# Optimization experiments

Measured on AMD Instinct MI355X. Metric: run time of the kernel, lower is better.

Reference implementation:

```python
import jax, jax.numpy as jnp
import numpy as np

D = 512
H = 8
DH = D // H


def setup_inputs() -> dict:
    key = jax.random.key(0)
    ks = jax.random.split(key, 6)
    B, S = 2, 4096
    scale = 1.0 / np.sqrt(D)
    x = jax.random.normal(ks[0], (B, S, D), dtype=jnp.float32)
    W_q = jax.random.normal(ks[1], (D, D), dtype=jnp.float32) * scale
    W_k = jax.random.normal(ks[2], (D, D), dtype=jnp.float32) * scale
    W_v = jax.random.normal(ks[3], (D, D), dtype=jnp.float32) * scale
    W_proj = jax.random.normal(ks[4], (D, D), dtype=jnp.float32) * scale
    b_proj = jax.random.normal(ks[5], (D,), dtype=jnp.float32) * 0.01
    return {"x": x, "W_q": W_q, "W_k": W_k, "W_v": W_v,
            "W_proj": W_proj, "b_proj": b_proj}


def reference(x, W_q, W_k, W_v, W_proj, b_proj):
    B, S, _ = x.shape
    # torch Linear: y = x @ W.T
    def proj(W):
        y = jnp.einsum('bsd,ed->bse', x, W)
        return y.reshape(B, S, H, DH).transpose(0, 2, 1, 3)  # [B,H,S,DH]
    q, k, v = proj(W_q), proj(W_k), proj(W_v)
    scores = jnp.einsum('bhqd,bhkd->bhqk', q, k) / np.sqrt(DH)  # [B,H,S,S]
    causal = jnp.tril(jnp.ones((S, S), dtype=bool))
    neg = jnp.finfo(scores.dtype).min
    scores = jnp.where(causal[None, None, :, :], scores, neg)
    w = jax.nn.softmax(scores, axis=-1)
    attn = jnp.einsum('bhqk,bhkd->bhqd', w, v)  # [B,H,S,DH]
    attn = attn.transpose(0, 2, 1, 3).reshape(B, S, D)
    return jnp.einsum('bsd,ed->bse', attn, W_proj) + b_proj
```

## Files before the change

kernel.cpp:

```cpp
#include <hip/hip_runtime.h>
#include <hip/hip_bf16.h>
#include <stdint.h>

#define D_MODEL 512
#define NH 8
#define DH 64
#define SEQ 4096
#define NBH 16
#define NX  (2 * SEQ * D_MODEL)
#define NW  (D_MODEL * D_MODEL)

typedef __attribute__((ext_vector_type(8))) short bf16x8;
typedef __attribute__((ext_vector_type(4))) float f32x4;
typedef __attribute__((ext_vector_type(16))) float f32x16;

#define CSCALE 0.18033688011112042f

__device__ __forceinline__ uint32_t pkbf(float a, float b) {
    uint32_t r;
    asm("v_cvt_pk_bf16_f32 %0, %1, %2" : "=v"(r) : "v"(a), "v"(b));
    return r;
}

#define SWZ(R) (((R) + ((R) >> 2)) & 3)

#define BAR() do {                                          \
    asm volatile("s_waitcnt lgkmcnt(0)" ::: "memory");      \
    __builtin_amdgcn_s_barrier();                           \
} while (0)

#define BARC(N) do {                                                     \
    asm volatile("s_waitcnt vmcnt(" #N ") lgkmcnt(0)" ::: "memory");     \
    __builtin_amdgcn_s_barrier();                                        \
} while (0)

typedef const __attribute__((address_space(1))) void* gvp;
typedef __attribute__((address_space(3))) void* lvp;
__device__ __forceinline__ void gload16(const short* g, short* l) {
    __builtin_amdgcn_global_load_lds((gvp)g, (lvp)l, 16, 0, 0);
}

__device__ __forceinline__ bf16x8 cvt8(float4 u, float4 v, float s) {
    union { uint32_t w[4]; bf16x8 h; } r;
    r.w[0] = pkbf(u.x * s, u.y * s); r.w[1] = pkbf(u.z * s, u.w * s);
    r.w[2] = pkbf(v.x * s, v.y * s); r.w[3] = pkbf(v.z * s, v.w * s);
    return r.h;
}

__global__ __launch_bounds__(256) void cvt_pre(
    const float* __restrict__ x,
    const float* __restrict__ Wq, const float* __restrict__ Wk,
    const float* __restrict__ Wv, const float* __restrict__ Wp,
    short* __restrict__ xb, short* __restrict__ Wb)
{
    const size_t t = ((size_t)blockIdx.x * 256 + threadIdx.x) * 8;
    const float* src; short* dst; float s = 1.0f; size_t off;
    if (t < NX) {
        src = x; dst = xb; off = t;
    } else {
        const size_t u = t - NX;
        const int w = (int)(u >> 18);
        off = u & (NW - 1);
        src = (w == 0) ? Wq : (w == 1) ? Wk : (w == 2) ? Wv : Wp;
        dst = Wb + ((size_t)w << 18);
        s = (w == 0) ? CSCALE : 1.0f;
    }
    float4 a = *(const float4*)(src + off);
    float4 b = *(const float4*)(src + off + 4);
    *(bf16x8*)(dst + off) = cvt8(a, b, s);
}

__global__ __launch_bounds__(256) void qkv_kernel(
    const short* __restrict__ xb, const short* __restrict__ Wb,
    short* __restrict__ Qb, short* __restrict__ Kb, short* __restrict__ Vt)
{
    __shared__ __align__(16) short at[3][4096];
    __shared__ __align__(16) short bt[3][4096];

    const int tid  = threadIdx.x;
    const int wave = tid >> 6;
    const int lane = tid & 63;
    const int ln = lane & 15, quad = lane >> 4;
    const int z = blockIdx.z;
    const short* W = Wb + ((size_t)z << 18);
    const int m0 = blockIdx.x * 128;
    const int n0 = blockIdx.y * 128;
    const int mh = (wave & 1) * 64, nh = (wave >> 1) * 64;

    const int ck0 = tid, ck1 = tid + 256;
    const int R0 = ck0 >> 2, R1 = ck1 >> 2;
    const int c0 = (ck0 & 3) ^ SWZ(R0), c1 = (ck1 & 3) ^ SWZ(R1);
    const int lbase = (tid & 192) * 8;

    auto stage = [&](int buf, int kc) {
        const short* gA0 = xb + (size_t)(m0 + R0) * D_MODEL + kc + c0 * 8;
        const short* gA1 = xb + (size_t)(m0 + R1) * D_MODEL + kc + c1 * 8;
        const short* gB0 = W + (size_t)(n0 + R0) * D_MODEL + kc + c0 * 8;
        const short* gB1 = W + (size_t)(n0 + R1) * D_MODEL + kc + c1 * 8;
        gload16(gA0, &at[buf][lbase]);
        gload16(gA1, &at[buf][lbase] + 2048);
        gload16(gB0, &bt[buf][lbase]);
        gload16(gB1, &bt[buf][lbase] + 2048);
    };

    f32x4 acc[4][4] = {};

    stage(0, 0);
    stage(1, 32);

    for (int s = 0; s < 16; ++s) {
        const int cur = s % 3;
        if (s == 15) BARC(0); else BARC(4);
        if (s < 14) stage((s + 2) % 3, (s + 2) * 32);

        bf16x8 a[4], b[4];
#pragma unroll
        for (int i = 0; i < 4; ++i) {
            const int R = mh + i * 16 + ln;
            a[i] = *(const bf16x8*)(&at[cur][R * 32 + ((quad ^ SWZ(R)) * 8)]);
        }
#pragma unroll
        for (int j = 0; j < 4; ++j) {
            const int R = nh + j * 16 + ln;
            b[j] = *(const bf16x8*)(&bt[cur][R * 32 + ((quad ^ SWZ(R)) * 8)]);
        }
        __builtin_amdgcn_s_setprio(1);
#pragma unroll
        for (int i = 0; i < 4; ++i)
#pragma unroll
            for (int j = 0; j < 4; ++j)
                acc[i][j] = __builtin_amdgcn_mfma_f32_16x16x32_bf16(
                    a[i], b[j], acc[i][j], 0, 0, 0);
        __builtin_amdgcn_s_setprio(0);
    }

    if (z == 2) {
#pragma unroll
        for (int i = 0; i < 4; ++i) {
            const int row0 = m0 + mh + i * 16 + quad * 4;
            const int bb = row0 >> 12, sq = row0 & (SEQ - 1);
#pragma unroll
            for (int j = 0; j < 4; ++j) {
                const int n = n0 + nh + j * 16 + ln;
                const int h = n >> 6, dh = n & 63;
                uint2 st;
                st.x = pkbf(acc[i][j][0], acc[i][j][1]);
                st.y = pkbf(acc[i][j][2], acc[i][j][3]);
                *(uint2*)(Vt + (size_t)((bb * NH + h) * DH + dh) * SEQ + sq) = st;
            }
        }
    } else {
        short* P = (z == 0) ? Qb : Kb;
#pragma unroll
        for (int i = 0; i < 4; ++i)
#pragma unroll
            for (int j = 0; j < 4; ++j) {
                const int n = n0 + nh + j * 16 + ln;
                const int h = n >> 6, dh = n & 63;
                const uint32_t lo = pkbf(acc[i][j][0], acc[i][j][1]);
                const uint32_t hi2 = pkbf(acc[i][j][2], acc[i][j][3]);
#pragma unroll
                for (int r = 0; r < 4; ++r) {
                    const int row = m0 + mh + i * 16 + quad * 4 + r;
                    const int bb = row >> 12, sq = row & (SEQ - 1);
                    const uint32_t w = (r < 2) ? lo : hi2;
                    P[((size_t)((bb * NH + h) * SEQ + sq) << 6) + dh] =
                        (short)((r & 1) ? (w >> 16) : (w & 0xffff));
                }
            }
    }
}

__global__ __launch_bounds__(256) void attn_kernel(
    const short* __restrict__ Qb, const short* __restrict__ Kb,
    const short* __restrict__ Vt, short* __restrict__ ao)
{
    __shared__ __align__(16) short kt[2][4096];
    __shared__ __align__(16) short vt[2][4096];

    const int tid  = threadIdx.x;
    const int wave = tid >> 6;
    const int lane = tid & 63;
    const int l31 = lane & 31, hi = lane >> 5;
    const int bh = blockIdx.y;
    const int w_ = (blockIdx.x + 4 * bh) & 31;
    const int g2 = ((bh >> 3) & 1) ? (31 - w_) : w_;
    const short* Qp = Qb + (size_t)bh * SEQ * DH;
    const short* Kp = Kb + (size_t)bh * SEQ * DH;
    const short* Vp = Vt + (size_t)bh * DH * SEQ;
    const int bb = bh >> 3, h = bh & 7;
    const int q0 = g2 * 128 + wave * 32;
    const int myq = q0 + l31;
    const int jdiag = q0 >> 6;
    const int jmax = 2 * g2 + 1;

    const int ckA = tid, ckB = tid + 256;
    const int RA = ckA >> 3, RB = ckB >> 3;
    const int cA = (ckA & 7) ^ (RA & 7), cB = (ckB & 7) ^ (RB & 7);
    const int RA31 = RA & 31, RB31 = RB & 31;
    const int kkA = (RA & 32) + ((RA31 & 8) << 1) + ((RA31 & 4) << 1)
                  + ((RA31 & 16) >> 2) + (RA31 & 3);
    const int kkB = (RB & 32) + ((RB31 & 8) << 1) + ((RB31 & 4) << 1)
                  + ((RB31 & 16) >> 2) + (RB31 & 3);
    const size_t kOffA = ((size_t)kkA << 6) + cA * 8;
    const size_t kOffB = ((size_t)kkB << 6) + cB * 8;
    const size_t vOffA = (size_t)RA * SEQ + cA * 8;
    const size_t vOffB = (size_t)RB * SEQ + cB * 8;

    bf16x8 sk0, sk1, sv0, sv1;
    auto load_tile = [&](int j) {
        const size_t k0 = (size_t)j * 64;
        sk0 = *(const bf16x8*)(Kp + (k0 << 6) + kOffA);
        sk1 = *(const bf16x8*)(Kp + (k0 << 6) + kOffB);
        sv0 = *(const bf16x8*)(Vp + vOffA + k0);
        sv1 = *(const bf16x8*)(Vp + vOffB + k0);
    };
    auto write_tile = [&](int buf) {
        *(bf16x8*)&kt[buf][ckA * 8] = sk0;
        *(bf16x8*)&kt[buf][ckB * 8] = sk1;
        *(bf16x8*)&vt[buf][ckA * 8] = sv0;
        *(bf16x8*)&vt[buf][ckB * 8] = sv1;
    };

    bf16x8 qf[4];
#pragma unroll
    for (int c = 0; c < 4; ++c)
        qf[c] = *(const bf16x8*)(Qp + (size_t)myq * DH + c * 16 + hi * 8);

    const bf16x8 ones = { (short)0x3F80, (short)0x3F80, (short)0x3F80,
                          (short)0x3F80, (short)0x3F80, (short)0x3F80,
                          (short)0x3F80, (short)0x3F80 };

    f32x16 o0 = {}, o1 = {};
    f32x16 lacc = {};

    load_tile(0);
    write_tile(0);
    load_tile(1);
    BAR();

    for (int j = 0; j <= jmax; ++j) {
        const int cur = j & 1;
        if (j < jmax) {
            write_tile(cur ^ 1);
            if (j + 1 < jmax) load_tile(j + 2);
        }

        if ((j << 6) <= q0 + 31) {
            f32x16 s0 = {}, s1 = {};
            const int sw = l31 & 7;
            __builtin_amdgcn_s_setprio(1);
#pragma unroll
            for (int c = 0; c < 4; ++c) {
                const int pc = ((2 * c + hi) ^ sw) * 8;
                bf16x8 a0 = *(const bf16x8*)(&kt[cur][l31 * 64 + pc]);
                bf16x8 a1 = *(const bf16x8*)(&kt[cur][(32 + l31) * 64 + pc]);
                s0 = __builtin_amdgcn_mfma_f32_32x32x16_bf16(a0, qf[c], s0, 0, 0, 0);
                s1 = __builtin_amdgcn_mfma_f32_32x32x16_bf16(a1, qf[c], s1, 0, 0, 0);
            }
            __builtin_amdgcn_s_setprio(0);
            if (j >= jdiag) {
                const int k0 = j * 64;
#pragma unroll
                for (int reg = 0; reg < 16; ++reg) {
                    const int kl = ((reg >> 2) & 1) * 16 + hi * 8
                                 + ((reg >> 3) & 1) * 4 + (reg & 3);
                    if (k0 + kl > myq)      s0[reg] = -3e38f;
                    if (k0 + 32 + kl > myq) s1[reg] = -3e38f;
                }
            }
#pragma unroll
            for (int i = 0; i < 16; ++i) {
                s0[i] = __builtin_amdgcn_exp2f(s0[i]);
                s1[i] = __builtin_amdgcn_exp2f(s1[i]);
            }

            union { uint32_t u[4]; bf16x8 v; } p00, p01, p10, p11;
            p00.u[0] = pkbf(s0[0], s0[1]);   p00.u[1] = pkbf(s0[2], s0[3]);
            p00.u[2] = pkbf(s0[8], s0[9]);   p00.u[3] = pkbf(s0[10], s0[11]);
            p01.u[0] = pkbf(s0[4], s0[5]);   p01.u[1] = pkbf(s0[6], s0[7]);
            p01.u[2] = pkbf(s0[12], s0[13]); p01.u[3] = pkbf(s0[14], s0[15]);
            p10.u[0] = pkbf(s1[0], s1[1]);   p10.u[1] = pkbf(s1[2], s1[3]);
            p10.u[2] = pkbf(s1[8], s1[9]);   p10.u[3] = pkbf(s1[10], s1[11]);
            p11.u[0] = pkbf(s1[4], s1[5]);   p11.u[1] = pkbf(s1[6], s1[7]);
            p11.u[2] = pkbf(s1[12], s1[13]); p11.u[3] = pkbf(s1[14], s1[15]);

            __builtin_amdgcn_s_setprio(1);
            lacc = __builtin_amdgcn_mfma_f32_32x32x16_bf16(ones, p00.v, lacc, 0, 0, 0);
            lacc = __builtin_amdgcn_mfma_f32_32x32x16_bf16(ones, p01.v, lacc, 0, 0, 0);
            lacc = __builtin_amdgcn_mfma_f32_32x32x16_bf16(ones, p10.v, lacc, 0, 0, 0);
            lacc = __builtin_amdgcn_mfma_f32_32x32x16_bf16(ones, p11.v, lacc, 0, 0, 0);

            {
                const short* vrow = &vt[cur][l31 * 64];
                bf16x8 v00 = *(const bf16x8*)(vrow + (((0 + hi) ^ sw) * 8));
                bf16x8 v01 = *(const bf16x8*)(vrow + (((2 + hi) ^ sw) * 8));
                bf16x8 v10 = *(const bf16x8*)(vrow + (((4 + hi) ^ sw) * 8));
                bf16x8 v11 = *(const bf16x8*)(vrow + (((6 + hi) ^ sw) * 8));
                o0 = __builtin_amdgcn_mfma_f32_32x32x16_bf16(v00, p00.v, o0, 0, 0, 0);
                o0 = __builtin_amdgcn_mfma_f32_32x32x16_bf16(v01, p01.v, o0, 0, 0, 0);
                o0 = __builtin_amdgcn_mfma_f32_32x32x16_bf16(v10, p10.v, o0, 0, 0, 0);
                o0 = __builtin_amdgcn_mfma_f32_32x32x16_bf16(v11, p11.v, o0, 0, 0, 0);
            }
            {
                const short* vrow = &vt[cur][(32 + l31) * 64];
                bf16x8 v00 = *(const bf16x8*)(vrow + (((0 + hi) ^ sw) * 8));
                bf16x8 v01 = *(const bf16x8*)(vrow + (((2 + hi) ^ sw) * 8));
                bf16x8 v10 = *(const bf16x8*)(vrow + (((4 + hi) ^ sw) * 8));
                bf16x8 v11 = *(const bf16x8*)(vrow + (((6 + hi) ^ sw) * 8));
                o1 = __builtin_amdgcn_mfma_f32_32x32x16_bf16(v00, p00.v, o1, 0, 0, 0);
                o1 = __builtin_amdgcn_mfma_f32_32x32x16_bf16(v01, p01.v, o1, 0, 0, 0);
                o1 = __builtin_amdgcn_mfma_f32_32x32x16_bf16(v10, p10.v, o1, 0, 0, 0);
                o1 = __builtin_amdgcn_mfma_f32_32x32x16_bf16(v11, p11.v, o1, 0, 0, 0);
            }
            __builtin_amdgcn_s_setprio(0);
        }
        BAR();
    }
    const float inv = 1.0f / lacc[0];
    short* orow = ao + (size_t)(bb * SEQ + myq) * D_MODEL + h * DH;
#pragma unroll
    for (int c = 0; c < 4; ++c) {
        uint2 st;
        st.x = pkbf(o0[4 * c] * inv,     o0[4 * c + 1] * inv);
        st.y = pkbf(o0[4 * c + 2] * inv, o0[4 * c + 3] * inv);
        *(uint2*)(orow + 8 * c + 4 * hi) = st;
    }
#pragma unroll
    for (int c = 0; c < 4; ++c) {
        uint2 st;
        st.x = pkbf(o1[4 * c] * inv,     o1[4 * c + 1] * inv);
        st.y = pkbf(o1[4 * c + 2] * inv, o1[4 * c + 3] * inv);
        *(uint2*)(orow + 32 + 8 * c + 4 * hi) = st;
    }
}

__global__ __launch_bounds__(256) void proj_kernel(
    const short* __restrict__ attn, const short* __restrict__ Wpb,
    const float* __restrict__ bias, float* __restrict__ out)
{
    __shared__ __align__(16) short at[3][2048];
    __shared__ __align__(16) short bt[3][4096];

    const int tid  = threadIdx.x;
    const int wave = tid >> 6;
    const int lane = tid & 63;
    const int ln = lane & 15, quad = lane >> 4;
    const int m0 = blockIdx.x * 64;
    const int n0 = blockIdx.y * 128;
    const int mh = (wave & 1) * 32, nh = (wave >> 1) * 64;

    const int RA = tid >> 2, cAc = (tid & 3) ^ SWZ(RA);
    const int ck0 = tid, ck1 = tid + 256;
    const int R0 = ck0 >> 2, R1 = ck1 >> 2;
    const int c0 = (ck0 & 3) ^ SWZ(R0), c1 = (ck1 & 3) ^ SWZ(R1);
    const int lbase = (tid & 192) * 8;

    auto stage = [&](int buf, int kc) {
        const short* gA = attn + (size_t)(m0 + RA) * D_MODEL + kc + cAc * 8;
        const short* gB0 = Wpb + (size_t)(n0 + R0) * D_MODEL + kc + c0 * 8;
        const short* gB1 = Wpb + (size_t)(n0 + R1) * D_MODEL + kc + c1 * 8;
        gload16(gA, &at[buf][lbase]);
        gload16(gB0, &bt[buf][lbase]);
        gload16(gB1, &bt[buf][lbase] + 2048);
    };

    f32x4 acc[2][4] = {};

    stage(0, 0);
    stage(1, 32);

    for (int s = 0; s < 16; ++s) {
        const int cur = s % 3;
        if (s == 15) BARC(0); else BARC(3);
        if (s < 14) stage((s + 2) % 3, (s + 2) * 32);

        bf16x8 a[2], b[4];
#pragma unroll
        for (int i = 0; i < 2; ++i) {
            const int R = mh + i * 16 + ln;
            a[i] = *(const bf16x8*)(&at[cur][R * 32 + ((quad ^ SWZ(R)) * 8)]);
        }
#pragma unroll
        for (int j = 0; j < 4; ++j) {
            const int R = nh + j * 16 + ln;
            b[j] = *(const bf16x8*)(&bt[cur][R * 32 + ((quad ^ SWZ(R)) * 8)]);
        }
        __builtin_amdgcn_s_setprio(1);
#pragma unroll
        for (int i = 0; i < 2; ++i)
#pragma unroll
            for (int j = 0; j < 4; ++j)
                acc[i][j] = __builtin_amdgcn_mfma_f32_16x16x32_bf16(
                    a[i], b[j], acc[i][j], 0, 0, 0);
        __builtin_amdgcn_s_setprio(0);
    }
#pragma unroll
    for (int j = 0; j < 4; ++j) {
        const int n = n0 + nh + j * 16 + ln;
        const float bv = bias[n];
#pragma unroll
        for (int i = 0; i < 2; ++i)
#pragma unroll
            for (int r = 0; r < 4; ++r) {
                const int row = m0 + mh + i * 16 + quad * 4 + r;
                out[(size_t)row * D_MODEL + n] = acc[i][j][r] + bv;
            }
    }
}

extern "C" void kernel_launch(void* const* d_in, const int* in_sizes, int n_in,
                              void* d_out, int out_size, void* d_ws, size_t ws_size,
                              hipStream_t stream) {
    const float* x  = (const float*)d_in[0];
    const float* Wq = (const float*)d_in[1];
    const float* Wk = (const float*)d_in[2];
    const float* Wv = (const float*)d_in[3];
    const float* Wp = (const float*)d_in[4];
    const float* bp = (const float*)d_in[5];
    float* out = (float*)d_out;

    short* Qb = (short*)d_ws;
    short* Kb = Qb + (size_t)NBH * SEQ * DH;
    short* Vt = Kb + (size_t)NBH * SEQ * DH;
    short* ab = Vt + (size_t)NBH * SEQ * DH;
    short* Wb = ab + (size_t)NBH * SEQ * DH;

    short* xb = (short*)d_out;

    cvt_pre<<<dim3((NX + 4 * NW) / (8 * 256)), 256, 0, stream>>>(
        x, Wq, Wk, Wv, Wp, xb, Wb);
    qkv_kernel<<<dim3(64, 4, 3), 256, 0, stream>>>(xb, Wb, Qb, Kb, Vt);
    attn_kernel<<<dim3(32, NBH), 256, 0, stream>>>(Qb, Kb, Vt, ab);
    proj_kernel<<<dim3(128, 4), 256, 0, stream>>>(ab, Wb + 3 * (size_t)NW, bp, out);
}
```

Baseline: 168.2 us.

## Merge paired query blocks into 512-thread attention blocks sharing K/V tiles

Attention blocks grow from 4 to 8 waves, each block covering two consecutive 128-query groups of one head. The K/V tiles staged in shared memory are reused by both groups, and each thread now loads one chunk instead of two. The intent is to halve global K/V traffic and load instructions per query. In exchange, the lower query group keeps iterating up to the upper group's causal limit, so its waves may stall at barriers or do masked work. The old reversed-ordering scheme used to balance causal work across blocks is dropped.

Measured after the change: 170.3 us. About the same (+1.3%).

```diff
diff --git a/kernel.cpp b/kernel.cpp
--- a/kernel.cpp
+++ b/kernel.cpp
@@ -171,7 +171,7 @@
     }
 }
 
-__global__ __launch_bounds__(256) void attn_kernel(
+__global__ __launch_bounds__(512) void attn_kernel(
     const short* __restrict__ Qb, const short* __restrict__ Kb,
     const short* __restrict__ Vt, short* __restrict__ ao)
 {
@@ -182,44 +182,39 @@
     const int wave = tid >> 6;
     const int lane = tid & 63;
     const int l31 = lane & 31, hi = lane >> 5;
-    const int bh = blockIdx.y;
-    const int w_ = (blockIdx.x + 4 * bh) & 31;
-    const int g2 = ((bh >> 3) & 1) ? (31 - w_) : w_;
+
+    const int bid = blockIdx.x + (blockIdx.y << 4);
+    const int bh  = bid & 15;
+    const int cp  = bid >> 4;
     const short* Qp = Qb + (size_t)bh * SEQ * DH;
     const short* Kp = Kb + (size_t)bh * SEQ * DH;
     const short* Vp = Vt + (size_t)bh * DH * SEQ;
     const int bb = bh >> 3, h = bh & 7;
-    const int q0 = g2 * 128 + wave * 32;
+
+    const int g2 = 2 * cp + (wave >> 2);
+    const int cw = wave & 3;
+    const int q0 = g2 * 128 + cw * 32;
     const int myq = q0 + l31;
     const int jdiag = q0 >> 6;
-    const int jmax = 2 * g2 + 1;
-
-    const int ckA = tid, ckB = tid + 256;
-    const int RA = ckA >> 3, RB = ckB >> 3;
-    const int cA = (ckA & 7) ^ (RA & 7), cB = (ckB & 7) ^ (RB & 7);
-    const int RA31 = RA & 31, RB31 = RB & 31;
+    const int jmax = 4 * cp + 3;
+
+    const int RA = tid >> 3;
+    const int cA = (tid & 7) ^ (RA & 7);
+    const int RA31 = RA & 31;
     const int kkA = (RA & 32) + ((RA31 & 8) << 1) + ((RA31 & 4) << 1)
                   + ((RA31 & 16) >> 2) + (RA31 & 3);
-    const int kkB = (RB & 32) + ((RB31 & 8) << 1) + ((RB31 & 4) << 1)
-                  + ((RB31 & 16) >> 2) + (RB31 & 3);
     const size_t kOffA = ((size_t)kkA << 6) + cA * 8;
-    const size_t kOffB = ((size_t)kkB << 6) + cB * 8;
     const size_t vOffA = (size_t)RA * SEQ + cA * 8;
-    const size_t vOffB = (size_t)RB * SEQ + cB * 8;
-
-    bf16x8 sk0, sk1, sv0, sv1;
+
+    bf16x8 sk0, sv0;
     auto load_tile = [&](int j) {
         const size_t k0 = (size_t)j * 64;
         sk0 = *(const bf16x8*)(Kp + (k0 << 6) + kOffA);
-        sk1 = *(const bf16x8*)(Kp + (k0 << 6) + kOffB);
         sv0 = *(const bf16x8*)(Vp + vOffA + k0);
-        sv1 = *(const bf16x8*)(Vp + vOffB + k0);
     };
     auto write_tile = [&](int buf) {
-        *(bf16x8*)&kt[buf][ckA * 8] = sk0;
-        *(bf16x8*)&kt[buf][ckB * 8] = sk1;
-        *(bf16x8*)&vt[buf][ckA * 8] = sv0;
-        *(bf16x8*)&vt[buf][ckB * 8] = sv1;
+        *(bf16x8*)&kt[buf][tid * 8] = sk0;
+        *(bf16x8*)&vt[buf][tid * 8] = sv0;
     };
 
     bf16x8 qf[4];
@@ -431,6 +426,6 @@
     cvt_pre<<<dim3((NX + 4 * NW) / (8 * 256)), 256, 0, stream>>>(
         x, Wq, Wk, Wv, Wp, xb, Wb);
     qkv_kernel<<<dim3(64, 4, 3), 256, 0, stream>>>(xb, Wb, Qb, Kb, Vt);
-    attn_kernel<<<dim3(32, NBH), 256, 0, stream>>>(Qb, Kb, Vt, ab);
+    attn_kernel<<<dim3(16, NBH), 512, 0, stream>>>(Qb, Kb, Vt, ab);
     proj_kernel<<<dim3(128, 4), 256, 0, stream>>>(ab, Wb + 3 * (size_t)NW, bp, out);
 }
```

## Fuse four pipeline stages into one persistent cooperative kernel with grid syncs

Applied to the files above, without the earlier changes.

Replaces four separate kernel launches (convert, QKV GEMM, attention, projection) with a single cooperative persistent kernel of 512 blocks that runs each stage in turn, separated by grid-wide syncs and sharing one LDS buffer. The goal is to remove launch overhead and inter-kernel gaps. In exchange, the grid size is fixed at 512 blocks, so the QKV stage needs two passes over its 768 tiles and the load is uneven, and grid.sync adds its own cost. If the cooperative launch fails, the code falls back to the original four launches.

Result: slower. 361.0 us (+114.6%).

```diff
diff --git a/kernel.cpp b/kernel.cpp
--- a/kernel.cpp
+++ b/kernel.cpp
@@ -1,6 +1,9 @@
 #include <hip/hip_runtime.h>
 #include <hip/hip_bf16.h>
+#include <hip/hip_cooperative_groups.h>
 #include <stdint.h>
+
+namespace cg = cooperative_groups;
 
 #define D_MODEL 512
 #define NH 8
@@ -47,13 +50,11 @@
     return r.h;
 }
 
-__global__ __launch_bounds__(256) void cvt_pre(
-    const float* __restrict__ x,
-    const float* __restrict__ Wq, const float* __restrict__ Wk,
-    const float* __restrict__ Wv, const float* __restrict__ Wp,
-    short* __restrict__ xb, short* __restrict__ Wb)
-{
-    const size_t t = ((size_t)blockIdx.x * 256 + threadIdx.x) * 8;
+
+__device__ __forceinline__ void cvt_body(
+    size_t t, const float* x, const float* Wq, const float* Wk,
+    const float* Wv, const float* Wp, short* xb, short* Wb)
+{
     const float* src; short* dst; float s = 1.0f; size_t off;
     if (t < NX) {
         src = x; dst = xb; off = t;
@@ -70,21 +71,16 @@
     *(bf16x8*)(dst + off) = cvt8(a, b, s);
 }
 
-__global__ __launch_bounds__(256) void qkv_kernel(
-    const short* __restrict__ xb, const short* __restrict__ Wb,
-    short* __restrict__ Qb, short* __restrict__ Kb, short* __restrict__ Vt)
-{
-    __shared__ __align__(16) short at[3][4096];
-    __shared__ __align__(16) short bt[3][4096];
-
-    const int tid  = threadIdx.x;
+__device__ __forceinline__ void qkv_body(
+    int m0, int n0, int z, int tid,
+    const short* xb, const short* Wb,
+    short* Qb, short* Kb, short* Vt,
+    short (*at)[4096], short (*bt)[4096])
+{
     const int wave = tid >> 6;
     const int lane = tid & 63;
     const int ln = lane & 15, quad = lane >> 4;
-    const int z = blockIdx.z;
     const short* W = Wb + ((size_t)z << 18);
-    const int m0 = blockIdx.x * 128;
-    const int n0 = blockIdx.y * 128;
     const int mh = (wave & 1) * 64, nh = (wave >> 1) * 64;
 
     const int ck0 = tid, ck1 = tid + 256;
@@ -171,20 +167,14 @@
     }
 }
 
-__global__ __launch_bounds__(256) void attn_kernel(
-    const short* __restrict__ Qb, const short* __restrict__ Kb,
-    const short* __restrict__ Vt, short* __restrict__ ao)
-{
-    __shared__ __align__(16) short kt[2][4096];
-    __shared__ __align__(16) short vt[2][4096];
-
-    const int tid  = threadIdx.x;
+__device__ __forceinline__ void attn_body(
+    int bh, int g2, int tid,
+    const short* Qb, const short* Kb, const short* Vt, short* ao,
+    short* kt0, short* vt0)
+{
     const int wave = tid >> 6;
     const int lane = tid & 63;
     const int l31 = lane & 31, hi = lane >> 5;
-    const int bh = blockIdx.y;
-    const int w_ = (blockIdx.x + 4 * bh) & 31;
-    const int g2 = ((bh >> 3) & 1) ? (31 - w_) : w_;
     const short* Qp = Qb + (size_t)bh * SEQ * DH;
     const short* Kp = Kb + (size_t)bh * SEQ * DH;
     const short* Vp = Vt + (size_t)bh * DH * SEQ;
@@ -216,10 +206,10 @@
         sv1 = *(const bf16x8*)(Vp + vOffB + k0);
     };
     auto write_tile = [&](int buf) {
-        *(bf16x8*)&kt[buf][ckA * 8] = sk0;
-        *(bf16x8*)&kt[buf][ckB * 8] = sk1;
-        *(bf16x8*)&vt[buf][ckA * 8] = sv0;
-        *(bf16x8*)&vt[buf][ckB * 8] = sv1;
+        *(bf16x8*)&kt0[buf * 4096 + ckA * 8] = sk0;
+        *(bf16x8*)&kt0[buf * 4096 + ckB * 8] = sk1;
+        *(bf16x8*)&vt0[buf * 4096 + ckA * 8] = sv0;
+        *(bf16x8*)&vt0[buf * 4096 + ckB * 8] = sv1;
     };
 
     bf16x8 qf[4];
@@ -253,8 +243,8 @@
 #pragma unroll
             for (int c = 0; c < 4; ++c) {
                 const int pc = ((2 * c + hi) ^ sw) * 8;
-                bf16x8 a0 = *(const bf16x8*)(&kt[cur][l31 * 64 + pc]);
-                bf16x8 a1 = *(const bf16x8*)(&kt[cur][(32 + l31) * 64 + pc]);
+                bf16x8 a0 = *(const bf16x8*)(&kt0[cur * 4096 + l31 * 64 + pc]);
+                bf16x8 a1 = *(const bf16x8*)(&kt0[cur * 4096 + (32 + l31) * 64 + pc]);
                 s0 = __builtin_amdgcn_mfma_f32_32x32x16_bf16(a0, qf[c], s0, 0, 0, 0);
                 s1 = __builtin_amdgcn_mfma_f32_32x32x16_bf16(a1, qf[c], s1, 0, 0, 0);
             }
@@ -292,7 +282,7 @@
             lacc = __builtin_amdgcn_mfma_f32_32x32x16_bf16(ones, p11.v, lacc, 0, 0, 0);
 
             {
-                const short* vrow = &vt[cur][l31 * 64];
+                const short* vrow = &vt0[cur * 4096 + l31 * 64];
                 bf16x8 v00 = *(const bf16x8*)(vrow + (((0 + hi) ^ sw) * 8));
                 bf16x8 v01 = *(const bf16x8*)(vrow + (((2 + hi) ^ sw) * 8));
                 bf16x8 v10 = *(const bf16x8*)(vrow + (((4 + hi) ^ sw) * 8));
@@ -303,7 +293,7 @@
                 o0 = __builtin_amdgcn_mfma_f32_32x32x16_bf16(v11, p11.v, o0, 0, 0, 0);
             }
             {
-                const short* vrow = &vt[cur][(32 + l31) * 64];
+                const short* vrow = &vt0[cur * 4096 + (32 + l31) * 64];
                 bf16x8 v00 = *(const bf16x8*)(vrow + (((0 + hi) ^ sw) * 8));
                 bf16x8 v01 = *(const bf16x8*)(vrow + (((2 + hi) ^ sw) * 8));
                 bf16x8 v10 = *(const bf16x8*)(vrow + (((4 + hi) ^ sw) * 8));
@@ -335,19 +325,14 @@
     }
 }
 
-__global__ __launch_bounds__(256) void proj_kernel(
-    const short* __restrict__ attn, const short* __restrict__ Wpb,
-    const float* __restrict__ bias, float* __restrict__ out)
-{
-    __shared__ __align__(16) short at[3][2048];
-    __shared__ __align__(16) short bt[3][4096];
-
-    const int tid  = threadIdx.x;
+__device__ __forceinline__ void proj_body(
+    int m0, int n0, int tid,
+    const short* ab, const short* Wpb, const float* bias, float* out,
+    short (*at)[2048], short (*bt)[4096])
+{
     const int wave = tid >> 6;
     const int lane = tid & 63;
     const int ln = lane & 15, quad = lane >> 4;
-    const int m0 = blockIdx.x * 64;
-    const int n0 = blockIdx.y * 128;
     const int mh = (wave & 1) * 32, nh = (wave >> 1) * 64;
 
     const int RA = tid >> 2, cAc = (tid & 3) ^ SWZ(RA);
@@ -357,7 +342,7 @@
     const int lbase = (tid & 192) * 8;
 
     auto stage = [&](int buf, int kc) {
-        const short* gA = attn + (size_t)(m0 + RA) * D_MODEL + kc + cAc * 8;
+        const short* gA = ab + (size_t)(m0 + RA) * D_MODEL + kc + cAc * 8;
         const short* gB0 = Wpb + (size_t)(n0 + R0) * D_MODEL + kc + c0 * 8;
         const short* gB1 = Wpb + (size_t)(n0 + R1) * D_MODEL + kc + c1 * 8;
         gload16(gA, &at[buf][lbase]);
@@ -407,6 +392,88 @@
                 out[(size_t)row * D_MODEL + n] = acc[i][j][r] + bv;
             }
     }
+}
+
+__global__ __launch_bounds__(256) void fused_kernel(
+    const float* x, const float* Wq, const float* Wk,
+    const float* Wv, const float* Wp, const float* bias,
+    short* xb, short* Wb, short* Qb, short* Kb, short* Vt,
+    short* ab, float* out)
+{
+    __shared__ __align__(16) short lds[24576];
+
+    cg::grid_group grid = cg::this_grid();
+    const int b   = blockIdx.x;
+    const int tid = threadIdx.x;
+
+    for (int i = 0; i < 5; ++i)
+        cvt_body(((size_t)(i * 512 + b) * 256 + tid) * 8,
+                 x, Wq, Wk, Wv, Wp, xb, Wb);
+    grid.sync();
+
+    for (int item = b; item < 768; item += 512) {
+        BAR();
+        qkv_body((item & 63) * 128, ((item >> 6) & 3) * 128, item >> 8,
+                 tid, xb, Wb, Qb, Kb, Vt,
+                 (short(*)[4096])lds, (short(*)[4096])(lds + 12288));
+    }
+    grid.sync();
+
+    {
+        const int bh = b >> 5;
+        const int w_ = ((b & 31) + 4 * bh) & 31;
+        const int g2 = ((bh >> 3) & 1) ? (31 - w_) : w_;
+        BAR();
+        attn_body(bh, g2, tid, Qb, Kb, Vt, ab, lds, lds + 8192);
+    }
+    grid.sync();
+
+    BAR();
+    proj_body((b >> 2) * 64, (b & 3) * 128, tid, ab, Wb + 3 * (size_t)NW,
+              bias, out,
+              (short(*)[2048])lds, (short(*)[4096])(lds + 6144));
+}
+
+__global__ __launch_bounds__(256) void cvt_pre(
+    const float* __restrict__ x,
+    const float* __restrict__ Wq, const float* __restrict__ Wk,
+    const float* __restrict__ Wv, const float* __restrict__ Wp,
+    short* xb, short* __restrict__ Wb)
+{
+    cvt_body(((size_t)blockIdx.x * 256 + threadIdx.x) * 8,
+             x, Wq, Wk, Wv, Wp, xb, Wb);
+}
+
+__global__ __launch_bounds__(256) void qkv_kernel(
+    const short* __restrict__ xb, const short* __restrict__ Wb,
+    short* __restrict__ Qb, short* __restrict__ Kb, short* __restrict__ Vt)
+{
+    __shared__ __align__(16) short at[3][4096];
+    __shared__ __align__(16) short bt[3][4096];
+    qkv_body(blockIdx.x * 128, blockIdx.y * 128, blockIdx.z,
+             threadIdx.x, xb, Wb, Qb, Kb, Vt, at, bt);
+}
+
+__global__ __launch_bounds__(256) void attn_kernel(
+    const short* __restrict__ Qb, const short* __restrict__ Kb,
+    const short* __restrict__ Vt, short* __restrict__ ao)
+{
+    __shared__ __align__(16) short kt[2][4096];
+    __shared__ __align__(16) short vt[2][4096];
+    const int bh = blockIdx.y;
+    const int w_ = (blockIdx.x + 4 * bh) & 31;
+    const int g2 = ((bh >> 3) & 1) ? (31 - w_) : w_;
+    attn_body(bh, g2, threadIdx.x, Qb, Kb, Vt, ao, &kt[0][0], &vt[0][0]);
+}
+
+__global__ __launch_bounds__(256) void proj_kernel(
+    const short* __restrict__ attn, const short* __restrict__ Wpb,
+    const float* __restrict__ bias, float* __restrict__ out)
+{
+    __shared__ __align__(16) short at[3][2048];
+    __shared__ __align__(16) short bt[3][4096];
+    proj_body(blockIdx.x * 64, blockIdx.y * 128, threadIdx.x,
+              attn, Wpb, bias, out, at, bt);
 }
 
 extern "C" void kernel_launch(void* const* d_in, const int* in_sizes, int n_in,
@@ -428,9 +495,19 @@
 
     short* xb = (short*)d_out;
 
-    cvt_pre<<<dim3((NX + 4 * NW) / (8 * 256)), 256, 0, stream>>>(
-        x, Wq, Wk, Wv, Wp, xb, Wb);
-    qkv_kernel<<<dim3(64, 4, 3), 256, 0, stream>>>(xb, Wb, Qb, Kb, Vt);
-    attn_kernel<<<dim3(32, NBH), 256, 0, stream>>>(Qb, Kb, Vt, ab);
-    proj_kernel<<<dim3(128, 4), 256, 0, stream>>>(ab, Wb + 3 * (size_t)NW, bp, out);
-}
+    void* args[] = { (void*)&x, (void*)&Wq, (void*)&Wk, (void*)&Wv,
+                     (void*)&Wp, (void*)&bp, (void*)&xb, (void*)&Wb,
+                     (void*)&Qb, (void*)&Kb, (void*)&Vt, (void*)&ab,
+                     (void*)&out };
+    hipError_t err = hipLaunchCooperativeKernel(
+        fused_kernel, dim3(512), dim3(256), args, 0, stream);
+
+    if (err != hipSuccess) {
+        cvt_pre<<<dim3((NX + 4 * NW) / (8 * 256)), 256, 0, stream>>>(
+            x, Wq, Wk, Wv, Wp, xb, Wb);
+        qkv_kernel<<<dim3(64, 4, 3), 256, 0, stream>>>(xb, Wb, Qb, Kb, Vt);
+        attn_kernel<<<dim3(32, NBH), 256, 0, stream>>>(Qb, Kb, Vt, ab);
+        proj_kernel<<<dim3(128, 4), 256, 0, stream>>>(ab, Wb + 3 * (size_t)NW,
+                                                      bp, out);
+    }
+}
```
